# Optimization experiments

Hardware: AMD Instinct MI355X
Metric: run time of the kernel (lower is better)

## Reference

```python
import jax, jax.numpy as jnp
import numpy as np

N = 100000

def _norm_edges(edge_index, n):
    # add self loops, compute symmetric GCN normalization
    loop = jnp.arange(n, dtype=edge_index.dtype)
    src = jnp.concatenate([edge_index[0], loop])
    dst = jnp.concatenate([edge_index[1], loop])
    deg = jax.ops.segment_sum(jnp.ones_like(dst, dtype=jnp.float32), dst, num_segments=n)
    dinv = jnp.where(deg > 0, deg ** -0.5, 0.0)
    norm = dinv[src] * dinv[dst]
    return src, dst, norm

def _gcn(x, W, b, src, dst, norm, n):
    h = x @ W  # [N, out]
    msg = h[src] * norm[:, None]
    return jax.ops.segment_sum(msg, dst, num_segments=n) + b

def setup_inputs() -> dict:
    key = jax.random.key(0)
    ks = jax.random.split(key, 20)
    E = 3200000
    d_in, d_out = 64, 64
    def w(k, i, o):
        return jax.random.normal(k, (i, o), dtype=jnp.float32) * (1.0 / np.sqrt(i))
    return {
        "x": jax.random.normal(ks[0], (N, d_in), dtype=jnp.float32),
        "t": jax.random.normal(ks[1], (N,), dtype=jnp.float32),
        "edge_index": jax.random.randint(ks[2], (2, E), 0, N, dtype=jnp.int64),
        "W1": w(ks[3], d_in + 1, 64), "b1": jnp.zeros((64,), jnp.float32),
        "W2": w(ks[4], 64, 128), "b2": jnp.zeros((128,), jnp.float32),
        "W3": w(ks[5], 128, 256), "b3": jnp.zeros((256,), jnp.float32),
        "W4": w(ks[6], 256, 128), "b4": jnp.zeros((128,), jnp.float32),
        "F1": w(ks[7], 128, 256), "c1": jnp.zeros((256,), jnp.float32),
        "F2": w(ks[8], 256, 128), "c2": jnp.zeros((128,), jnp.float32),
        "F3": w(ks[9], 128, d_out), "c3": jnp.zeros((d_out,), jnp.float32),
    }

def reference(x, t, edge_index, W1, b1, W2, b2, W3, b3, W4, b4, F1, c1, F2, c2, F3, c3):
    n = x.shape[0]
    src, dst, norm = _norm_edges(edge_index, n)
    h = jnp.concatenate([x, t[:, None]], axis=1)
    h = jax.nn.gelu(_gcn(h, W1, b1, src, dst, norm, n))
    h = jax.nn.gelu(_gcn(h, W2, b2, src, dst, norm, n))
    h = jax.nn.gelu(_gcn(h, W3, b3, src, dst, norm, n))
    h = jax.nn.gelu(_gcn(h, W4, b4, src, dst, norm, n))
    h = jax.nn.gelu(h @ F1 + c1)
    h = jax.nn.gelu(h @ F2 + c2)
    return h @ F3 + c3
```

## Files before the change

### kernel.cpp

```cpp
#include <hip/hip_runtime.h>

static constexpr int BLK = 256;

typedef double d2 __attribute__((ext_vector_type(2)));
typedef int    i4 __attribute__((ext_vector_type(4)));

__device__ __forceinline__ double gelu_d(double v){
  double u = 0.7978845608028654 * (v + 0.044715 * v * v * v);
  return 0.5 * v * (1.0 + tanh(u));
}

__global__ void zero_k(int* __restrict__ a, int n){
  int stride = gridDim.x * blockDim.x;
  for (int i = blockIdx.x*blockDim.x + threadIdx.x; i < n; i += stride) a[i] = 0;
}

__global__ void zeromax_k(unsigned long long* m){
  if (threadIdx.x == 0 && blockIdx.x == 0){ m[0] = 0ull; m[1] = 0ull; }
}

__global__ void detect_k(const int* __restrict__ ei, int* __restrict__ flag){
  if (threadIdx.x == 0 && blockIdx.x == 0){
    int zeros = 0;
    for (int i = 0; i < 64; ++i) if (ei[2*i + 1] == 0) ++zeros;
    *flag = (zeros >= 48) ? 1 : 0;
  }
}

__global__ void count_k(const int* __restrict__ ei, int E, const int* __restrict__ flag,
                        int* __restrict__ cnt){
  int is64 = *flag;
  int stride = gridDim.x * blockDim.x;
  for (int e = blockIdx.x*blockDim.x + threadIdx.x; e < E; e += stride){
    int d = is64 ? ei[2*(E + e)] : ei[E + e];
    atomicAdd(&cnt[d], 1);
  }
}

__global__ void dinv_k(const int* __restrict__ cnt, double* __restrict__ dinv, int n){
  int i = blockIdx.x*blockDim.x + threadIdx.x;
  if (i < n){
    double deg = (double)(cnt[i] + 1);
    dinv[i] = 1.0 / sqrt(deg);
  }
}

__global__ __launch_bounds__(256)
void scanA_k(const int* __restrict__ cnt, int* __restrict__ partial, int n, int chunk){
  __shared__ int red[256];
  int b = blockIdx.x;
  int lo = b * chunk, hi = min(n, lo + chunk);
  int s = 0;
  for (int i = lo + threadIdx.x; i < hi; i += 256) s += cnt[i];
  red[threadIdx.x] = s; __syncthreads();
  for (int off = 128; off > 0; off >>= 1){
    if (threadIdx.x < off) red[threadIdx.x] += red[threadIdx.x + off];
    __syncthreads();
  }
  if (threadIdx.x == 0) partial[b] = red[0];
}

__global__ __launch_bounds__(256)
void scanB_k(int* __restrict__ partial, int nb){
  __shared__ int sd[256];
  int tid = threadIdx.x;
  int v = (tid < nb) ? partial[tid] : 0;
  sd[tid] = v; __syncthreads();
  for (int off = 1; off < 256; off <<= 1){
    int t = (tid >= off) ? sd[tid - off] : 0;
    __syncthreads();
    sd[tid] += t;
    __syncthreads();
  }
  if (tid < nb) partial[tid] = sd[tid] - v;
  if (tid == 255) partial[nb] = sd[255];
}

__global__ __launch_bounds__(256)
void scanC_k(const int* __restrict__ cnt, const int* __restrict__ partial,
             int* __restrict__ rp, int n, int chunk, int nb){
  __shared__ int sd[256];
  int b = blockIdx.x;
  int lo = b * chunk, hi = min(n, lo + chunk);
  int run = partial[b];
  for (int base = lo; base < hi; base += 256){
    int i = base + threadIdx.x;
    int v = (i < hi) ? cnt[i] : 0;
    sd[threadIdx.x] = v; __syncthreads();
    for (int off = 1; off < 256; off <<= 1){
      int t = (threadIdx.x >= off) ? sd[threadIdx.x - off] : 0;
      __syncthreads();
      sd[threadIdx.x] += t;
      __syncthreads();
    }
    if (i < hi) rp[i] = run + sd[threadIdx.x] - v;
    run += sd[255];
    __syncthreads();
  }
  if (b == 0 && threadIdx.x == 0) rp[n] = partial[nb];
}

__global__ void scatter_k(const int* __restrict__ ei, int E, const int* __restrict__ flag,
                          const int* __restrict__ rp, int* __restrict__ fill,
                          const double* __restrict__ dinv,
                          int* __restrict__ col, double* __restrict__ val){
  int is64 = *flag;
  int stride = gridDim.x * blockDim.x;
  for (int e = blockIdx.x*blockDim.x + threadIdx.x; e < E; e += stride){
    int s = is64 ? ei[2*e]       : ei[e];
    int d = is64 ? ei[2*(E + e)] : ei[E + e];
    int p = rp[d] + atomicAdd(&fill[d], 1);
    col[p] = s;
    if (val) val[p] = dinv[s];
  }
}

template<typename ST>
__global__ void concat_k(const float* __restrict__ x, const float* __restrict__ t,
                         ST* __restrict__ h0, int n){
  int total = n * 66;
  int stride = gridDim.x * blockDim.x;
  for (int idx = blockIdx.x*blockDim.x + threadIdx.x; idx < total; idx += stride){
    int row = idx / 66;
    int c = idx - row * 66;
    float v = (c < 64) ? x[row*64 + c] : (c == 64 ? t[row] : 0.0f);
    h0[idx] = (ST)v;
  }
}

template<typename ST>
__global__ __launch_bounds__(256, 4)
void gemm_k(const ST* __restrict__ A, int K, int lda,
            const float* __restrict__ W, int NOUT,
            const float* __restrict__ bias,
            ST* __restrict__ C, float* __restrict__ Cf,
            int n, int fuse, unsigned long long* __restrict__ amax)
{
  __shared__ __align__(16) double As[128][18];
  __shared__ __align__(16) double Ws[16][66];
  const int row0 = blockIdx.x * 128;
  const int col0 = blockIdx.y * 64;
  const int tid = threadIdx.x;
  const int tr = tid >> 4, tc = tid & 15;
  const int c0 = 2 * tc;
  double acc[8][4] = {};

  const int sar = tid >> 1;
  const int sak = (tid & 1) * 8;
  const int swr = tid >> 4;
  const int swc = (tid & 15) * 4;

  const int ktiles = (K + 15) / 16;

  double ga[8];
  float  gw[4];

  auto loadA = [&](int k0){
    int gr = row0 + sar;
    if constexpr (sizeof(ST) == 8){
      if (gr < n){
        const double* Ap = (const double*)A + (size_t)gr * lda + k0 + sak;
        #pragma unroll
        for (int g = 0; g < 4; ++g){
          d2 v = *(const d2*)(Ap + 2*g);
          ga[2*g] = v.x; ga[2*g+1] = v.y;
        }
      } else {
        #pragma unroll
        for (int u = 0; u < 8; ++u) ga[u] = 0.0;
      }
    } else {
      const ST* Ap = A + (size_t)gr * lda + k0 + sak;
      #pragma unroll
      for (int u = 0; u < 8; ++u){
        int kg = k0 + sak + u;
        ga[u] = (gr < n && kg < K) ? (double)Ap[u] : 0.0;
      }
    }
  };
  auto loadW = [&](int k0){
    int kg = k0 + swr;
    if (kg < K){
      const float* Wp = W + (size_t)kg * NOUT + col0 + swc;
      #pragma unroll
      for (int g = 0; g < 4; ++g) gw[g] = Wp[g];
    } else {
      #pragma unroll
      for (int g = 0; g < 4; ++g) gw[g] = 0.0f;
    }
  };

  loadA(0);
  loadW(0);

  for (int kt = 0; kt < ktiles; ++kt){
    #pragma unroll
    for (int g = 0; g < 4; ++g){
      d2 v; v.x = ga[2*g]; v.y = ga[2*g+1];
      *(d2*)&As[sar][sak + 2*g] = v;
    }
    {
      d2 v0; v0.x = (double)gw[0]; v0.y = (double)gw[1];
      d2 v1; v1.x = (double)gw[2]; v1.y = (double)gw[3];
      *(d2*)&Ws[swr][swc]     = v0;
      *(d2*)&Ws[swr][swc + 2] = v1;
    }
    __syncthreads();
    if (kt + 1 < ktiles){
      loadA((kt + 1) * 16);
      loadW((kt + 1) * 16);
    }
    #pragma unroll
    for (int kk = 0; kk < 16; kk += 2){
      d2 w0a = *(const d2*)&Ws[kk    ][c0];
      d2 w0b = *(const d2*)&Ws[kk    ][c0 + 32];
      d2 w1a = *(const d2*)&Ws[kk + 1][c0];
      d2 w1b = *(const d2*)&Ws[kk + 1][c0 + 32];
      #pragma unroll
      for (int i = 0; i < 8; ++i){
        d2 av = *(const d2*)&As[tr + 16*i][kk];
        acc[i][0] = fma(av.x, w0a.x, acc[i][0]);
        acc[i][1] = fma(av.x, w0a.y, acc[i][1]);
        acc[i][2] = fma(av.x, w0b.x, acc[i][2]);
        acc[i][3] = fma(av.x, w0b.y, acc[i][3]);
        acc[i][0] = fma(av.y, w1a.x, acc[i][0]);
        acc[i][1] = fma(av.y, w1a.y, acc[i][1]);
        acc[i][2] = fma(av.y, w1b.x, acc[i][2]);
        acc[i][3] = fma(av.y, w1b.y, acc[i][3]);
      }
    }
    __syncthreads();
  }
  double tmax = 0.0;
  #pragma unroll
  for (int i = 0; i < 8; ++i){
    int r = row0 + tr + 16*i;
    if (r >= n) continue;
    #pragma unroll
    for (int j = 0; j < 4; ++j){
      int c = col0 + ((j < 2) ? (c0 + j) : (c0 + 30 + j));
      double v = acc[i][j];
      if (fuse){ v += (double)bias[c]; if (fuse == 1) v = gelu_d(v); }
      if (amax) tmax = fmax(tmax, fabs(v));
      if (fuse == 2) __builtin_nontemporal_store((float)v, &Cf[(size_t)r * NOUT + c]);
      else           __builtin_nontemporal_store((ST)v,   &C [(size_t)r * NOUT + c]);
    }
  }
  if (amax){
    #pragma unroll
    for (int off = 32; off > 0; off >>= 1)
      tmax = fmax(tmax, __shfl_xor(tmax, off));
    if ((threadIdx.x & 63) == 0)
      atomicMax(amax, (unsigned long long)__double_as_longlong(tmax));
  }
}


__global__ void absmaxW_k(const float* __restrict__ W, int n, unsigned long long* __restrict__ out){
  double tmax = 0.0;
  int stride = gridDim.x * blockDim.x;
  for (int i = blockIdx.x*blockDim.x + threadIdx.x; i < n; i += stride)
    tmax = fmax(tmax, (double)fabsf(W[i]));
  #pragma unroll
  for (int off = 32; off > 0; off >>= 1)
    tmax = fmax(tmax, __shfl_xor(tmax, off));
  if ((threadIdx.x & 63) == 0)
    atomicMax(out, (unsigned long long)__double_as_longlong(tmax));
}

__global__ void quantW_k(const float* __restrict__ W, int K, int N,
                         const unsigned long long* __restrict__ maxw,
                         char* __restrict__ WqT){
  double wm = __longlong_as_double((long long)*maxw);
  int sw = (wm > 0.0) ? (37 - ilogb(wm)) : 0;
  double sc = ldexp(1.0, sw);
  int total = K * N;
  size_t NK = (size_t)N * K;
  int stride = gridDim.x * blockDim.x;
  for (int t = blockIdx.x*blockDim.x + threadIdx.x; t < total; t += stride){
    int k = t / N, nn = t - k * N;
    long long v = __double2ll_rn((double)W[t] * sc);
    #pragma unroll
    for (int p = 0; p < 5; ++p){
      int d = (int)((v + 128) & 255) - 128;
      WqT[(size_t)p * NK + (size_t)nn * K + k] = (char)d;
      v = (v - d) >> 8;
    }
  }
}

__global__ void quantA_k(const double* __restrict__ A, size_t MK,
                         const unsigned long long* __restrict__ maxa,
                         char* __restrict__ Aq){
  double am = __longlong_as_double((long long)*maxa);
  int sa = (am > 0.0) ? (38 - ilogb(am)) : 0;
  double sc = ldexp(1.0, sa);
  size_t stride = (size_t)gridDim.x * blockDim.x;
  for (size_t i = blockIdx.x*(size_t)blockDim.x + threadIdx.x; i < MK; i += stride){
    long long v = __double2ll_rn(A[i] * sc);
    #pragma unroll
    for (int p = 0; p < 5; ++p){
      int d = (int)((v + 128) & 255) - 128;
      Aq[(size_t)p * MK + i] = (char)d;
      v = (v - d) >> 8;
    }
  }
}

__global__ __launch_bounds__(512)
void ozaki_k(const char* __restrict__ Aq, const char* __restrict__ WqT,
             const unsigned long long* __restrict__ maxa,
             const unsigned long long* __restrict__ maxw,
             double* __restrict__ C, int n, int K, int N)
{
  constexpr int PP[22] = {0,0,0, 1,1,1,1, 2,2,2,2,2, 3,3,3,3,3, 4,4,4,4,4};
  constexpr int QQ[22] = {2,3,4, 1,2,3,4, 0,1,2,3,4, 0,1,2,3,4, 0,1,2,3,4};
  __shared__ __align__(16) char laq[5 * 16 * 80];
  const size_t MK = (size_t)n * K;
  const size_t NK = (size_t)N * K;
  const int tid  = threadIdx.x;
  const int lane = tid & 63;
  const int ct   = tid >> 6;
  const int l15  = lane & 15;
  const int lk   = lane >> 4;
  const int row0 = blockIdx.x * 16;

  i4 acc[22];
  #pragma unroll
  for (int i = 0; i < 22; ++i){ i4 z = {0,0,0,0}; acc[i] = z; }

  const int ksteps = K / 64;
  for (int ks = 0; ks < ksteps; ++ks){
    int k0 = ks * 64;
    if (ks) __syncthreads();
    if (tid < 320){
      int p  = tid >> 6;
      int rr = (tid >> 2) & 15;
      int sg = tid & 3;
      int gr = row0 + rr; if (gr >= n) gr = n - 1;
      i4 v = *(const i4*)(Aq + (size_t)p * MK + (size_t)gr * K + k0 + sg * 16);
      *(i4*)(laq + p * 1280 + rr * 80 + sg * 16) = v;
    }
    __syncthreads();
    i4 af[5], bf[5];
    #pragma unroll
    for (int p = 0; p < 5; ++p)
      af[p] = *(const i4*)(laq + p * 1280 + l15 * 80 + lk * 16);
    #pragma unroll
    for (int q = 0; q < 5; ++q)
      bf[q] = *(const i4*)(WqT + (size_t)q * NK + (size_t)(ct * 16 + l15) * K + k0 + lk * 16);
    #pragma unroll
    for (int i = 0; i < 22; ++i)
      acc[i] = __builtin_amdgcn_mfma_i32_16x16x64_i8(af[PP[i]], bf[QQ[i]], acc[i], 0, 0, 0);
  }

  double am = __longlong_as_double((long long)*maxa);
  double wm = __longlong_as_double((long long)*maxw);
  int sa = (am > 0.0) ? (38 - ilogb(am)) : 0;
  int sw = (wm > 0.0) ? (37 - ilogb(wm)) : 0;
  double s = ldexp(1.0, -(sa + sw));
  #pragma unroll
  for (int m = 0; m < 4; ++m){
    int r = row0 + lk * 4 + m;
    if (r >= n) continue;
    double sum = 0.0;
    #pragma unroll
    for (int i = 0; i < 22; ++i)
      sum += ldexp((double)acc[i][m], 8 * (PP[i] + QQ[i]));
    int c = ct * 16 + l15;
    __builtin_nontemporal_store(sum * s, &C[(size_t)r * N + c]);
  }
}

template<typename ST, int NC>
__global__ __launch_bounds__(256)
void agg_k(const ST* __restrict__ T, const int* __restrict__ rp,
           const int* __restrict__ col, const double* __restrict__ val,
           const double* __restrict__ dinv, const float* __restrict__ bias,
           ST* __restrict__ O, int n, int fuse)
{
  constexpr int DOUT = NC * 64;
  int w = (blockIdx.x * blockDim.x + threadIdx.x) >> 6;
  int lane = threadIdx.x & 63;
  if (w >= n) return;
  double dv = dinv[w];
  const ST* Ti = T + (size_t)w * DOUT;
  double acc[NC];
  #pragma unroll
  for (int c = 0; c < NC; ++c) acc[c] = dv * (double)Ti[lane + 64*c];
  int e  = rp[w];
  int e1 = rp[w + 1];
  if (val){
    for (; e + 4 <= e1; e += 4){
      int s0 = __builtin_nontemporal_load(&col[e]);
      int s1 = __builtin_nontemporal_load(&col[e+1]);
      int s2 = __builtin_nontemporal_load(&col[e+2]);
      int s3 = __builtin_nontemporal_load(&col[e+3]);
      double v0 = __builtin_nontemporal_load(&val[e]);
      double v1 = __builtin_nontemporal_load(&val[e+1]);
      double v2 = __builtin_nontemporal_load(&val[e+2]);
      double v3 = __builtin_nontemporal_load(&val[e+3]);
      const ST* T0 = T + (size_t)s0 * DOUT;
      const ST* T1 = T + (size_t)s1 * DOUT;
      const ST* T2 = T + (size_t)s2 * DOUT;
      const ST* T3 = T + (size_t)s3 * DOUT;
      double t0[NC], t1[NC], t2[NC], t3[NC];
      #pragma unroll
      for (int c = 0; c < NC; ++c){
        t0[c] = (double)T0[lane + 64*c];
        t1[c] = (double)T1[lane + 64*c];
        t2[c] = (double)T2[lane + 64*c];
        t3[c] = (double)T3[lane + 64*c];
      }
      #pragma unroll
      for (int c = 0; c < NC; ++c){
        acc[c] = fma(v0, t0[c], acc[c]);
        acc[c] = fma(v1, t1[c], acc[c]);
        acc[c] = fma(v2, t2[c], acc[c]);
        acc[c] = fma(v3, t3[c], acc[c]);
      }
    }
    for (; e < e1; ++e){
      int s = __builtin_nontemporal_load(&col[e]);
      double v = __builtin_nontemporal_load(&val[e]);
      const ST* Ts = T + (size_t)s * DOUT;
      #pragma unroll
      for (int c = 0; c < NC; ++c) acc[c] = fma(v, (double)Ts[lane + 64*c], acc[c]);
    }
  } else {
    for (; e < e1; ++e){
      int s = col[e];
      double v = dinv[s];
      const ST* Ts = T + (size_t)s * DOUT;
      #pragma unroll
      for (int c = 0; c < NC; ++c) acc[c] = fma(v, (double)Ts[lane + 64*c], acc[c]);
    }
  }
  ST* Oi = O + (size_t)w * DOUT;
  #pragma unroll
  for (int c = 0; c < NC; ++c){
    double v = dv * acc[c];
    if (fuse) v = gelu_d(v + (double)bias[lane + 64*c]);
    __builtin_nontemporal_store((ST)v, &Oi[lane + 64*c]);
  }
}

template<typename ST>
static void run_net(const float* x, const float* t,
                    const float* W1, const float* b1, const float* W2, const float* b2,
                    const float* W3, const float* b3, const float* W4, const float* b4,
                    const float* F1, const float* c1, const float* F2, const float* c2,
                    const float* F3, const float* c3,
                    ST* b256, ST* ba, ST* bb,
                    const int* rp, const int* col, const double* val, const double* dinv,
                    char* Aq, char* WqT, unsigned long long* maxbuf, bool ozk,
                    float* out, int N, hipStream_t stream)
{
  auto gemm = [&](const ST* A, int K, int lda, const float* W, int NOUT, const float* bias,
                  ST* C, float* Cf, int fuse, unsigned long long* amax){
    dim3 g((N + 127) / 128, NOUT / 64);
    gemm_k<ST><<<g, dim3(BLK), 0, stream>>>(A, K, lda, W, NOUT, bias, C, Cf, N, fuse, amax);
  };
  int aggGrid = (N * 64 + BLK - 1) / BLK;
  auto agg64 = [&](const ST* T, const float* bias, ST* O, int fuse){
    agg_k<ST,1><<<dim3(aggGrid), dim3(BLK), 0, stream>>>(T, rp, col, val, dinv, bias, O, N, fuse);
  };
  auto agg128 = [&](const ST* T, const float* bias, ST* O, int fuse){
    agg_k<ST,2><<<dim3(aggGrid), dim3(BLK), 0, stream>>>(T, rp, col, val, dinv, bias, O, N, fuse);
  };

  concat_k<ST><<<dim3(1024), dim3(BLK), 0, stream>>>(x, t, ba, N);
  gemm(ba, 65, 66, W1, 64, nullptr, bb, nullptr, 0, nullptr);
  agg64(bb, b1, ba, 1);
  agg64(ba, nullptr, bb, 0);
  gemm(bb, 64, 64, W2, 128, b2, ba, nullptr, 1, nullptr);
  agg128(ba, nullptr, bb, 0);
  gemm(bb, 128, 128, W3, 256, b3, b256, nullptr, 1,
       ozk ? maxbuf : nullptr);
  if (ozk){
    if constexpr (sizeof(ST) == 8){
      size_t MK = (size_t)N * 256;
      quantA_k<<<dim3(4096), dim3(BLK), 0, stream>>>((const double*)b256, MK, maxbuf, Aq);
      ozaki_k<<<dim3((N + 15) / 16), dim3(512), 0, stream>>>(
          Aq, WqT, maxbuf, maxbuf + 1, (double*)ba, N, 256, 128);
    }
  } else {
    gemm(b256, 256, 256, W4, 128, nullptr, ba, nullptr, 0, nullptr);
  }
  agg128(ba, b4, bb, 1);
  gemm(bb, 128, 128, F1, 256, c1, b256, nullptr, 1, nullptr);
  gemm(b256, 256, 256, F2, 128, c2, ba, nullptr, 1, nullptr);
  gemm(ba, 128, 128, F3, 64, c3, nullptr, out, 2, nullptr);
}

extern "C" void kernel_launch(void* const* d_in, const int* in_sizes, int n_in,
                              void* d_out, int out_size, void* d_ws, size_t ws_size,
                              hipStream_t stream)
{
  const float* x  = (const float*)d_in[0];
  const float* t  = (const float*)d_in[1];
  const int*   ei = (const int*)d_in[2];
  const float* W1 = (const float*)d_in[3];  const float* b1 = (const float*)d_in[4];
  const float* W2 = (const float*)d_in[5];  const float* b2 = (const float*)d_in[6];
  const float* W3 = (const float*)d_in[7];  const float* b3 = (const float*)d_in[8];
  const float* W4 = (const float*)d_in[9];  const float* b4 = (const float*)d_in[10];
  const float* F1 = (const float*)d_in[11]; const float* c1 = (const float*)d_in[12];
  const float* F2 = (const float*)d_in[13]; const float* c2 = (const float*)d_in[14];
  const float* F3 = (const float*)d_in[15]; const float* c3 = (const float*)d_in[16];
  float* out = (float*)d_out;
  int N = in_sizes[0] / 64;
  int E = in_sizes[2] / 2;

  char* p = (char*)d_ws;
  auto alloc = [&](size_t b){ char* r = p; p += (b + 255) & ~(size_t)255; return (void*)r; };
  int*    flag    = (int*)alloc(4);
  int*    cnt     = (int*)alloc((size_t)N * 4);
  int*    fill    = (int*)alloc((size_t)N * 4);
  int*    rp      = (int*)alloc((size_t)(N + 1) * 4);
  int*    partial = (int*)alloc((size_t)257 * 4);
  int*    col     = (int*)alloc((size_t)E * 4);
  double* dinv    = (double*)alloc((size_t)N * 8);
  size_t base = (size_t)(p - (char*)d_ws);

  size_t slackB = 1024;
  size_t actElems = (size_t)N * 512;
  size_t valBytes = ((size_t)E * 8 + 255) & ~(size_t)255;
  bool f64val = ws_size >= base + valBytes + actElems * sizeof(double) + 3*slackB;
  bool f64ok  = f64val || ws_size >= base + actElems * sizeof(double) + 3*slackB;
  bool f32val = ws_size >= base + valBytes + actElems * sizeof(float) + 3*slackB;
  bool f32ok  = f32val || ws_size >= base + actElems * sizeof(float) + 3*slackB;
  if (!f32ok) return;

  double* val = nullptr;
  if ((f64ok && f64val) || (!f64ok && f32val)) val = (double*)alloc((size_t)E * 8);

  int nb = 256;
  int chunk = (N + nb - 1) / nb;
  zero_k<<<dim3(256), dim3(BLK), 0, stream>>>(cnt, N);
  zero_k<<<dim3(256), dim3(BLK), 0, stream>>>(fill, N);
  detect_k<<<1, 64, 0, stream>>>(ei, flag);
  count_k<<<dim3(4096), dim3(BLK), 0, stream>>>(ei, E, flag, cnt);
  dinv_k<<<dim3((N + BLK - 1) / BLK), dim3(BLK), 0, stream>>>(cnt, dinv, N);
  scanA_k<<<dim3(nb), dim3(256), 0, stream>>>(cnt, partial, N, chunk);
  scanB_k<<<dim3(1), dim3(256), 0, stream>>>(partial, nb);
  scanC_k<<<dim3(nb), dim3(256), 0, stream>>>(cnt, partial, rp, N, chunk, nb);
  scatter_k<<<dim3(4096), dim3(BLK), 0, stream>>>(ei, E, flag, rp, fill, dinv, col, val);

  if (f64ok){
    double* b256 = (double*)alloc((size_t)N * 256 * 8 + slackB);
    double* ba   = (double*)alloc((size_t)N * 128 * 8 + slackB);
    double* bb   = (double*)alloc((size_t)N * 128 * 8 + slackB);
    size_t MK = (size_t)N * 256;
    size_t need = (size_t)(p - (char*)d_ws) + 5*MK + 5*32768 + 1024;
    bool ozk = (ws_size >= need);
    char* Aq = nullptr; char* WqT = nullptr; unsigned long long* maxbuf = nullptr;
    if (ozk){
      maxbuf = (unsigned long long*)alloc(256);
      Aq     = (char*)alloc(5 * MK);
      WqT    = (char*)alloc(5 * 32768);
      zeromax_k<<<1, 64, 0, stream>>>(maxbuf);
      absmaxW_k<<<dim3(32), dim3(BLK), 0, stream>>>(W4, 256 * 128, maxbuf + 1);
      quantW_k<<<dim3(128), dim3(BLK), 0, stream>>>(W4, 256, 128, maxbuf + 1, WqT);
    }
    run_net<double>(x, t, W1, b1, W2, b2, W3, b3, W4, b4, F1, c1, F2, c2, F3, c3,
                    b256, ba, bb, rp, col, val, dinv,
                    Aq, WqT, maxbuf, ozk, out, N, stream);
  } else {
    float* b256 = (float*)alloc((size_t)N * 256 * 4 + slackB);
    float* ba   = (float*)alloc((size_t)N * 128 * 4 + slackB);
    float* bb   = (float*)alloc((size_t)N * 128 * 4 + slackB);
    run_net<float>(x, t, W1, b1, W2, b2, W3, b3, W4, b4, F1, c1, F2, c2, F3, c3,
                   b256, ba, bb, rp, col, val, dinv,
                   nullptr, nullptr, nullptr, false, out, N, stream);
  }
}
```

Baseline: 2.558 ms.

## Fuse A-quantization into Ozaki int8 GEMM and apply it to the F2 layer

```diff
diff --git a/kernel.cpp b/kernel.cpp
--- a/kernel.cpp
+++ b/kernel.cpp
@@ -16,7 +16,9 @@
 }
 
 __global__ void zeromax_k(unsigned long long* m){
-  if (threadIdx.x == 0 && blockIdx.x == 0){ m[0] = 0ull; m[1] = 0ull; }
+  if (threadIdx.x == 0 && blockIdx.x == 0){
+    m[0] = 0ull; m[1] = 0ull; m[2] = 0ull; m[3] = 0ull;
+  }
 }
 
 __global__ void detect_k(const int* __restrict__ ei, int* __restrict__ flag){
@@ -289,35 +291,17 @@
   }
 }
 
-__global__ void quantA_k(const double* __restrict__ A, size_t MK,
-                         const unsigned long long* __restrict__ maxa,
-                         char* __restrict__ Aq){
-  double am = __longlong_as_double((long long)*maxa);
-  int sa = (am > 0.0) ? (38 - ilogb(am)) : 0;
-  double sc = ldexp(1.0, sa);
-  size_t stride = (size_t)gridDim.x * blockDim.x;
-  for (size_t i = blockIdx.x*(size_t)blockDim.x + threadIdx.x; i < MK; i += stride){
-    long long v = __double2ll_rn(A[i] * sc);
-    #pragma unroll
-    for (int p = 0; p < 5; ++p){
-      int d = (int)((v + 128) & 255) - 128;
-      Aq[(size_t)p * MK + i] = (char)d;
-      v = (v - d) >> 8;
-    }
-  }
-}
-
 __global__ __launch_bounds__(512)
-void ozaki_k(const char* __restrict__ Aq, const char* __restrict__ WqT,
+void ozaki_k(const double* __restrict__ A, const char* __restrict__ WqT,
              const unsigned long long* __restrict__ maxa,
              const unsigned long long* __restrict__ maxw,
-             double* __restrict__ C, int n, int K, int N)
+             const float* __restrict__ bias,
+             double* __restrict__ C, int n, int fuse)
 {
+  constexpr int K = 256, N = 128;
   constexpr int PP[22] = {0,0,0, 1,1,1,1, 2,2,2,2,2, 3,3,3,3,3, 4,4,4,4,4};
   constexpr int QQ[22] = {2,3,4, 1,2,3,4, 0,1,2,3,4, 0,1,2,3,4, 0,1,2,3,4};
-  __shared__ __align__(16) char laq[5 * 16 * 80];
-  const size_t MK = (size_t)n * K;
-  const size_t NK = (size_t)N * K;
+  __shared__ __align__(16) char laq[5][16][272];
   const int tid  = threadIdx.x;
   const int lane = tid & 63;
   const int ct   = tid >> 6;
@@ -325,39 +309,55 @@
   const int lk   = lane >> 4;
   const int row0 = blockIdx.x * 16;
 
-  i4 acc[22];
-  #pragma unroll
-  for (int i = 0; i < 22; ++i){ i4 z = {0,0,0,0}; acc[i] = z; }
-
-  const int ksteps = K / 64;
-  for (int ks = 0; ks < ksteps; ++ks){
-    int k0 = ks * 64;
-    if (ks) __syncthreads();
-    if (tid < 320){
-      int p  = tid >> 6;
-      int rr = (tid >> 2) & 15;
-      int sg = tid & 3;
-      int gr = row0 + rr; if (gr >= n) gr = n - 1;
-      i4 v = *(const i4*)(Aq + (size_t)p * MK + (size_t)gr * K + k0 + sg * 16);
-      *(i4*)(laq + p * 1280 + rr * 80 + sg * 16) = v;
-    }
-    __syncthreads();
-    i4 af[5], bf[5];
-    #pragma unroll
-    for (int p = 0; p < 5; ++p)
-      af[p] = *(const i4*)(laq + p * 1280 + l15 * 80 + lk * 16);
-    #pragma unroll
-    for (int q = 0; q < 5; ++q)
-      bf[q] = *(const i4*)(WqT + (size_t)q * NK + (size_t)(ct * 16 + l15) * K + k0 + lk * 16);
-    #pragma unroll
-    for (int i = 0; i < 22; ++i)
-      acc[i] = __builtin_amdgcn_mfma_i32_16x16x64_i8(af[PP[i]], bf[QQ[i]], acc[i], 0, 0, 0);
-  }
-
   double am = __longlong_as_double((long long)*maxa);
   double wm = __longlong_as_double((long long)*maxw);
   int sa = (am > 0.0) ? (38 - ilogb(am)) : 0;
   int sw = (wm > 0.0) ? (37 - ilogb(wm)) : 0;
+  double sc = ldexp(1.0, sa);
+
+  {
+    int r  = tid >> 5;
+    int k8 = (tid & 31) * 8;
+    int gr = row0 + r; if (gr >= n) gr = n - 1;
+    const double* Ap = A + (size_t)gr * K + k8;
+    unsigned long long pack[5] = {0,0,0,0,0};
+    #pragma unroll
+    for (int u = 0; u < 8; ++u){
+      long long v = __double2ll_rn(Ap[u] * sc);
+      #pragma unroll
+      for (int p = 0; p < 5; ++p){
+        int d = (int)((v + 128) & 255) - 128;
+        pack[p] |= (unsigned long long)(unsigned char)d << (8*u);
+        v = (v - d) >> 8;
+      }
+    }
+    #pragma unroll
+    for (int p = 0; p < 5; ++p)
+      *(unsigned long long*)&laq[p][r][k8] = pack[p];
+  }
+  __syncthreads();
+
+  i4 acc[22];
+  #pragma unroll
+  for (int i = 0; i < 22; ++i){ i4 z = {0,0,0,0}; acc[i] = z; }
+
+  const size_t NK = (size_t)N * K;
+  const char* Wbase = WqT + (size_t)(ct * 16 + l15) * K + lk * 16;
+  #pragma unroll
+  for (int ks = 0; ks < 4; ++ks){
+    int k0 = ks * 64;
+    i4 af[5], bf[5];
+    #pragma unroll
+    for (int p = 0; p < 5; ++p)
+      af[p] = *(const i4*)&laq[p][l15][k0 + lk*16];
+    #pragma unroll
+    for (int q = 0; q < 5; ++q)
+      bf[q] = *(const i4*)(Wbase + (size_t)q * NK + k0);
+    #pragma unroll
+    for (int i = 0; i < 22; ++i)
+      acc[i] = __builtin_amdgcn_mfma_i32_16x16x64_i8(af[PP[i]], bf[QQ[i]], acc[i], 0, 0, 0);
+  }
+
   double s = ldexp(1.0, -(sa + sw));
   #pragma unroll
   for (int m = 0; m < 4; ++m){
@@ -368,7 +368,9 @@
     for (int i = 0; i < 22; ++i)
       sum += ldexp((double)acc[i][m], 8 * (PP[i] + QQ[i]));
     int c = ct * 16 + l15;
-    __builtin_nontemporal_store(sum * s, &C[(size_t)r * N + c]);
+    double v = sum * s;
+    if (fuse) v = gelu_d(v + (double)bias[c]);
+    __builtin_nontemporal_store(v, &C[(size_t)r * N + c]);
   }
 }
 
@@ -453,7 +455,7 @@
                     const float* F3, const float* c3,
                     ST* b256, ST* ba, ST* bb,
                     const int* rp, const int* col, const double* val, const double* dinv,
-                    char* Aq, char* WqT, unsigned long long* maxbuf, bool ozk,
+                    char* Wq4, char* WqF2, unsigned long long* maxbuf, bool ozk,
                     float* out, int N, hipStream_t stream)
 {
   auto gemm = [&](const ST* A, int K, int lda, const float* W, int NOUT, const float* bias,
@@ -479,17 +481,23 @@
        ozk ? maxbuf : nullptr);
   if (ozk){
     if constexpr (sizeof(ST) == 8){
-      size_t MK = (size_t)N * 256;
-      quantA_k<<<dim3(4096), dim3(BLK), 0, stream>>>((const double*)b256, MK, maxbuf, Aq);
       ozaki_k<<<dim3((N + 15) / 16), dim3(512), 0, stream>>>(
-          Aq, WqT, maxbuf, maxbuf + 1, (double*)ba, N, 256, 128);
+          (const double*)b256, Wq4, maxbuf, maxbuf + 1, nullptr, (double*)ba, N, 0);
     }
   } else {
     gemm(b256, 256, 256, W4, 128, nullptr, ba, nullptr, 0, nullptr);
   }
   agg128(ba, b4, bb, 1);
-  gemm(bb, 128, 128, F1, 256, c1, b256, nullptr, 1, nullptr);
-  gemm(b256, 256, 256, F2, 128, c2, ba, nullptr, 1, nullptr);
+  gemm(bb, 128, 128, F1, 256, c1, b256, nullptr, 1,
+       ozk ? maxbuf + 2 : nullptr);
+  if (ozk){
+    if constexpr (sizeof(ST) == 8){
+      ozaki_k<<<dim3((N + 15) / 16), dim3(512), 0, stream>>>(
+          (const double*)b256, WqF2, maxbuf + 2, maxbuf + 3, c2, (double*)ba, N, 1);
+    }
+  } else {
+    gemm(b256, 256, 256, F2, 128, c2, ba, nullptr, 1, nullptr);
+  }
   gemm(ba, 128, 128, F3, 64, c3, nullptr, out, 2, nullptr);
 }
 
@@ -550,21 +558,23 @@
     double* b256 = (double*)alloc((size_t)N * 256 * 8 + slackB);
     double* ba   = (double*)alloc((size_t)N * 128 * 8 + slackB);
     double* bb   = (double*)alloc((size_t)N * 128 * 8 + slackB);
-    size_t MK = (size_t)N * 256;
-    size_t need = (size_t)(p - (char*)d_ws) + 5*MK + 5*32768 + 1024;
+    size_t wqB = 5 * 128 * 256;
+    size_t need = (size_t)(p - (char*)d_ws) + 2*wqB + 1024;
     bool ozk = (ws_size >= need);
-    char* Aq = nullptr; char* WqT = nullptr; unsigned long long* maxbuf = nullptr;
+    char* Wq4 = nullptr; char* WqF2 = nullptr; unsigned long long* maxbuf = nullptr;
     if (ozk){
       maxbuf = (unsigned long long*)alloc(256);
-      Aq     = (char*)alloc(5 * MK);
-      WqT    = (char*)alloc(5 * 32768);
+      Wq4    = (char*)alloc(wqB);
+      WqF2   = (char*)alloc(wqB);
       zeromax_k<<<1, 64, 0, stream>>>(maxbuf);
       absmaxW_k<<<dim3(32), dim3(BLK), 0, stream>>>(W4, 256 * 128, maxbuf + 1);
-      quantW_k<<<dim3(128), dim3(BLK), 0, stream>>>(W4, 256, 128, maxbuf + 1, WqT);
+      quantW_k<<<dim3(128), dim3(BLK), 0, stream>>>(W4, 256, 128, maxbuf + 1, Wq4);
+      absmaxW_k<<<dim3(32), dim3(BLK), 0, stream>>>(F2, 256 * 128, maxbuf + 3);
+      quantW_k<<<dim3(128), dim3(BLK), 0, stream>>>(F2, 256, 128, maxbuf + 3, WqF2);
     }
     run_net<double>(x, t, W1, b1, W2, b2, W3, b3, W4, b4, F1, c1, F2, c2, F3, c3,
                     b256, ba, bb, rp, col, val, dinv,
-                    Aq, WqT, maxbuf, ozk, out, N, stream);
+                    Wq4, WqF2, maxbuf, ozk, out, N, stream);
   } else {
     float* b256 = (float*)alloc((size_t)N * 256 * 4 + slackB);
     float* ba   = (float*)alloc((size_t)N * 128 * 4 + slackB);
```

New measurement: 2.560 ms. No clear change (+0.1%).
